# Kernel optimization log

Hardware: AMD Instinct MI355X
Metric: run time of the kernel (lower is better)

## Reference

```python
import jax, jax.numpy as jnp
import numpy as np

B, S, D_MODEL, N_HEADS = 4, 2048, 1024, 16
HEAD_DIM = D_MODEL // N_HEADS  # 64; used only for the softmax scale, as in the source


def setup_inputs() -> dict:
    key = jax.random.key(0)
    kq, kk, kv, kw = jax.random.split(key, 4)
    q = jax.random.normal(kq, (B, S, D_MODEL), dtype=jnp.float32)
    k = jax.random.normal(kk, (B, S, D_MODEL), dtype=jnp.float32)
    v = jax.random.normal(kv, (B, S, D_MODEL), dtype=jnp.float32)
    # out_proj: nn.Linear(d_model, d_model, bias=False) -> weight [out, in]
    W_out = jax.random.normal(kw, (D_MODEL, D_MODEL), dtype=jnp.float32) * (1.0 / np.sqrt(D_MODEL))
    return {"q": q, "k": k, "v": v, "W_out": W_out}


def reference(q, k, v, W_out):
    scale = 1.0 / jnp.sqrt(jnp.float32(HEAD_DIM))
    # scores: [B, Sq, Sk] -- full quadratic score matrix, as in the source
    scores = jnp.einsum("bqd,bkd->bqk", q, k) * scale
    attn = jax.nn.softmax(scores, axis=-1)
    out = jnp.einsum("bqk,bkd->bqd", attn, v)
    # torch Linear: y = x @ W^T
    return jnp.einsum("bsd,ed->bse", out, W_out)
```

## Files before the change

### kernel.cpp

```cpp
#include <hip/hip_runtime.h>
#include <hip/hip_fp16.h>
#include <stdint.h>

typedef _Float16 h16;
typedef _Float16 h16x8 __attribute__((ext_vector_type(8)));
typedef float f32x4 __attribute__((ext_vector_type(4)));

#define BB 4
#define SS 2048
#define DD 1024

#define EPI_H16 0
#define EPI_DIV 2

__device__ __forceinline__ void gload16(const void* g, void* l) {
    __builtin_amdgcn_global_load_lds(
        (const __attribute__((address_space(1))) uint32_t*)g,
        (__attribute__((address_space(3))) uint32_t*)l, 16, 0, 0);
}

__global__ __launch_bounds__(256) void cvt_qk(
    const float* __restrict__ q, const float* __restrict__ k,
    h16* __restrict__ qh, h16* __restrict__ kh, float* __restrict__ rowsum) {
    if (blockIdx.x == 0) {
#pragma unroll
        for (int i = 0; i < 32; ++i) rowsum[threadIdx.x + i * 256] = 0.f;
    }
    int b = blockIdx.x;
    const float* src; h16* dst; float sc = 1.0f;
    if (b < 1024)      { src = q; dst = qh; sc = 0.125f; }
    else               { src = k; dst = kh; b -= 1024; }
    size_t base = (size_t)b * 2048 + threadIdx.x;
    float4 a[8];
#pragma unroll
    for (int i = 0; i < 8; ++i) a[i] = ((const float4*)src)[base + (size_t)i * 256];
#pragma unroll
    for (int i = 0; i < 8; ++i) {
        union { int2 i2; h16 h[4]; } u;
        u.h[0] = (h16)(a[i].x * sc); u.h[1] = (h16)(a[i].y * sc);
        u.h[2] = (h16)(a[i].z * sc); u.h[3] = (h16)(a[i].w * sc);
        ((int2*)dst)[base + (size_t)i * 256] = u.i2;
    }
}

__device__ __forceinline__ void cvt_store(h16* dst, size_t g, float4 a) {
    union { int2 i2; h16 h[4]; } u;
    u.h[0] = (h16)a.x; u.h[1] = (h16)a.y; u.h[2] = (h16)a.z; u.h[3] = (h16)a.w;
    ((int2*)dst)[g] = u.i2;
}

__global__ __launch_bounds__(512, 2) void gemm1f(
    const h16* __restrict__ A, const h16* __restrict__ B, h16* __restrict__ C,
    const float* __restrict__ v, const float* __restrict__ w,
    h16* __restrict__ vh, h16* __restrict__ wh, float* __restrict__ rowsum)
{
    constexpr int ABYTES = 256 * 128;
    constexpr int BUFB   = 2 * ABYTES;
    __shared__ __align__(1024) char lds[2 * BUFB];

    const int tid = threadIdx.x;
    const int gid = blockIdx.x;
    const size_t tidg = (size_t)gid * 512 + tid;

    const int wgid = (gid & 7) * 32 + (gid >> 3);
    const int bb  = wgid / 64;
    const int rem = wgid % 64;
    const int tm = rem / 8, tn = rem % 8;
    const int row0 = tm * 256, col0 = tn * 256;

    const h16* Ab = A + (long long)bb * ((long long)SS * DD);
    const h16* Bb = B + (long long)bb * ((long long)SS * DD);

    const int lane = tid & 63, wid = tid >> 6;
    const int wm = wid >> 2, wn = wid & 3;
    const int frow = lane & 15, kq = lane >> 4;

    const int NT = DD >> 6;

    f32x4 acc[8][4];
#pragma unroll
    for (int m = 0; m < 8; ++m)
#pragma unroll
        for (int n = 0; n < 4; ++n) acc[m][n] = (f32x4){0.f, 0.f, 0.f, 0.f};

    char* l0 = (char*)lds;

    auto STAGE_B = [&](int kt, int buf) {
#pragma unroll
        for (int i = 0; i < 4; ++i) {
            int d = i * 512 + tid;
            int s = d & 7, r = d >> 3;
            int gg = s ^ (r & 7);
            gload16(Bb + (size_t)(col0 + r) * DD + kt + gg * 8,
                    l0 + buf * BUFB + ABYTES + (r * 8 + s) * 16);
        }
    };
    auto STAGE_AH = [&](int kt, int buf, int mh) {
#pragma unroll
        for (int i = 0; i < 2; ++i) {
            int d = i * 512 + tid;
            int s = d & 7, hr = d >> 3;
            int r = ((hr & ~63) << 1) + mh * 64 + (hr & 63);
            int gg = s ^ (r & 7);
            gload16(Ab + (size_t)(row0 + r) * DD + kt + gg * 8,
                    l0 + buf * BUFB + (r * 8 + s) * 16);
        }
    };
    auto READ_A = [&](int buf, int mh, h16x8 (&af)[4][2]) {
#pragma unroll
        for (int mm = 0; mm < 4; ++mm)
#pragma unroll
            for (int ks = 0; ks < 2; ++ks) {
                int r = wm * 128 + (mh * 4 + mm) * 16 + frow;
                int s = (ks * 4 + kq) ^ (r & 7);
                af[mm][ks] = *(const h16x8*)(l0 + buf * BUFB + (r * 8 + s) * 16);
            }
    };
    auto READ_B = [&](int buf, h16x8 (&bf)[4][2]) {
#pragma unroll
        for (int nn = 0; nn < 4; ++nn)
#pragma unroll
            for (int ks = 0; ks < 2; ++ks) {
                int r = wn * 64 + nn * 16 + frow;
                int s = (ks * 4 + kq) ^ (r & 7);
                bf[nn][ks] = *(const h16x8*)(l0 + buf * BUFB + ABYTES + (r * 8 + s) * 16);
            }
    };
    auto MFMA_H = [&](int mh, h16x8 (&af)[4][2], h16x8 (&bf)[4][2]) {
        __builtin_amdgcn_s_setprio(1);
#pragma unroll
        for (int ks = 0; ks < 2; ++ks)
#pragma unroll
            for (int mm = 0; mm < 4; ++mm)
#pragma unroll
                for (int nn = 0; nn < 4; ++nn)
                    acc[mh * 4 + mm][nn] =
                        __builtin_amdgcn_mfma_f32_16x16x32_f16(
                            af[mm][ks], bf[nn][ks], acc[mh * 4 + mm][nn], 0, 0, 0);
        __builtin_amdgcn_s_setprio(0);
    };

    {
        float4 w0 = ((const float4*)w)[tidg];
        float4 w1 = ((const float4*)w)[131072 + tidg];
        cvt_store(wh, tidg, w0);
        cvt_store(wh, 131072 + tidg, w1);
    }
    STAGE_B(0, 0); STAGE_AH(0, 0, 0); STAGE_AH(0, 0, 1);
    asm volatile("s_waitcnt vmcnt(2)" ::: "memory");
    __builtin_amdgcn_s_barrier();

    h16x8 af[4][2], bf[4][2];
    float4 vbuf;

    for (int G = 0; G < NT; ++G) {
        const int buf = G & 1;
        const int kt1 = (G + 1) << 6;
        float4 vnew = ((const float4*)v)[(size_t)G * 131072 + tidg];
        if (G > 0) cvt_store(vh, (size_t)(G - 1) * 131072 + tidg, vbuf);
        vbuf = vnew;
        if (G + 1 < NT) {
            STAGE_B(kt1, buf ^ 1);
            STAGE_AH(kt1, buf ^ 1, 0);
            STAGE_AH(kt1, buf ^ 1, 1);
        }
        READ_A(buf, 0, af);
        READ_B(buf, bf);
        MFMA_H(0, af, bf);
        if (G + 1 < NT) asm volatile("s_waitcnt vmcnt(8)" ::: "memory");
        else            asm volatile("s_waitcnt vmcnt(0)" ::: "memory");
        __builtin_amdgcn_s_barrier();
        READ_A(buf, 1, af);
        MFMA_H(1, af, bf);
        if (G + 1 >= NT) break;
        asm volatile("s_waitcnt vmcnt(2)" ::: "memory");
        __builtin_amdgcn_s_barrier();
    }
    cvt_store(vh, (size_t)(NT - 1) * 131072 + tidg, vbuf);

    h16* Cb = C + (long long)bb * ((long long)SS * SS);
    float* rs = rowsum + bb * SS;
    const int erow = row0 + wm * 128 + (lane >> 4) * 4;
    const int ecol = col0 + wn * 64 + (lane & 15);
#pragma unroll
    for (int m = 0; m < 8; ++m)
#pragma unroll
        for (int j = 0; j < 4; ++j) {
            const int row = erow + m * 16 + j;
            float p = 0.f;
#pragma unroll
            for (int n = 0; n < 4; ++n) {
                float e = __expf(acc[m][n][j] - 16.0f);
                Cb[(size_t)row * SS + (ecol + n * 16)] = (h16)e;
                p += e;
            }
            p += __shfl_xor(p, 1);
            p += __shfl_xor(p, 2);
            p += __shfl_xor(p, 4);
            p += __shfl_xor(p, 8);
            if ((lane & 15) == 0) atomicAdd(&rs[row], p);
        }
}

template<int EPI>
__global__ __launch_bounds__(256, 2) void gemm2p_sm(
    const h16* __restrict__ A, const h16* __restrict__ B, void* __restrict__ Cv,
    int lda, int ldb, int ldc, int K, int tilesN, int tilesMN,
    long long aBatch, long long bBatch, long long cBatch, const float* __restrict__ rowsum)
{
    constexpr int ABYTES = 128 * 128;
    constexpr int BBYTES = 128 * 128;
    constexpr int BUFB   = ABYTES + BBYTES;

    __shared__ __align__(1024) char lds[2 * BUFB];

    const int tid = threadIdx.x;
    const int nwg = gridDim.x;
    const int bid = blockIdx.x;
    const int wgid = (bid & 7) * (nwg >> 3) + (bid >> 3);
    const int bb  = wgid / tilesMN;
    const int rem = wgid % tilesMN;
    const int tm = rem / tilesN, tn = rem % tilesN;
    const int row0 = tm * 128, col0 = tn * 128;

    const h16* Ab = A + (long long)bb * aBatch;
    const h16* Bb = B + (long long)bb * bBatch;

    const int lane = tid & 63, wid = tid >> 6;
    const int wm = wid >> 1, wn = wid & 1;
    const int frow = lane & 15, kq = lane >> 4;

    const int NT = K >> 6;

    f32x4 acc[4][4];
#pragma unroll
    for (int m = 0; m < 4; ++m)
#pragma unroll
        for (int n = 0; n < 4; ++n) acc[m][n] = (f32x4){0.f, 0.f, 0.f, 0.f};

    char* l0 = (char*)lds;

    auto STAGE_B = [&](int kt, int buf) {
#pragma unroll
        for (int i = 0; i < 4; ++i) {
            int d = i * 256 + tid;
            int s = d & 7, r = d >> 3;
            int gg = s ^ (r & 7);
            gload16(Bb + (size_t)(col0 + r) * ldb + kt + gg * 8,
                    l0 + buf * BUFB + ABYTES + (r * 8 + s) * 16);
        }
    };
    auto STAGE_AH = [&](int kt, int buf, int mh) {
#pragma unroll
        for (int i = 0; i < 2; ++i) {
            int d = i * 256 + tid;
            int s = d & 7, hr = d >> 3;
            int r = ((hr & ~31) << 1) + mh * 32 + (hr & 31);
            int gg = s ^ (r & 7);
            gload16(Ab + (size_t)(row0 + r) * lda + kt + gg * 8,
                    l0 + buf * BUFB + (r * 8 + s) * 16);
        }
    };
    auto READ_A = [&](int buf, int mh, h16x8 (&af)[2][2]) {
#pragma unroll
        for (int mm = 0; mm < 2; ++mm)
#pragma unroll
            for (int ks = 0; ks < 2; ++ks) {
                int r = wm * 64 + (mh * 2 + mm) * 16 + frow;
                int s = (ks * 4 + kq) ^ (r & 7);
                af[mm][ks] = *(const h16x8*)(l0 + buf * BUFB + (r * 8 + s) * 16);
            }
    };
    auto READ_B = [&](int buf, h16x8 (&bf)[4][2]) {
#pragma unroll
        for (int nn = 0; nn < 4; ++nn)
#pragma unroll
            for (int ks = 0; ks < 2; ++ks) {
                int r = wn * 64 + nn * 16 + frow;
                int s = (ks * 4 + kq) ^ (r & 7);
                bf[nn][ks] = *(const h16x8*)(l0 + buf * BUFB + ABYTES + (r * 8 + s) * 16);
            }
    };
    auto MFMA_H = [&](int mh, h16x8 (&af)[2][2], h16x8 (&bf)[4][2]) {
        __builtin_amdgcn_s_setprio(1);
#pragma unroll
        for (int ks = 0; ks < 2; ++ks)
#pragma unroll
            for (int mm = 0; mm < 2; ++mm)
#pragma unroll
                for (int nn = 0; nn < 4; ++nn)
                    acc[mh * 2 + mm][nn] =
                        __builtin_amdgcn_mfma_f32_16x16x32_f16(
                            af[mm][ks], bf[nn][ks], acc[mh * 2 + mm][nn], 0, 0, 0);
        __builtin_amdgcn_s_setprio(0);
    };

    STAGE_B(0, 0); STAGE_AH(0, 0, 0); STAGE_AH(0, 0, 1);
    asm volatile("s_waitcnt vmcnt(2)" ::: "memory");
    __builtin_amdgcn_s_barrier();

    h16x8 af[2][2], bf[4][2];

    for (int G = 0; G < NT; ++G) {
        const int buf = G & 1;
        const int kt1 = (G + 1) << 6;
        if (G + 1 < NT) {
            STAGE_B(kt1, buf ^ 1);
            STAGE_AH(kt1, buf ^ 1, 0);
            STAGE_AH(kt1, buf ^ 1, 1);
        }
        READ_A(buf, 0, af);
        READ_B(buf, bf);
        MFMA_H(0, af, bf);
        if (G + 1 < NT) asm volatile("s_waitcnt vmcnt(8)" ::: "memory");
        else            asm volatile("s_waitcnt vmcnt(0)" ::: "memory");
        __builtin_amdgcn_s_barrier();
        READ_A(buf, 1, af);
        MFMA_H(1, af, bf);
        if (G + 1 >= NT) break;
        asm volatile("s_waitcnt vmcnt(2)" ::: "memory");
        __builtin_amdgcn_s_barrier();
    }

    const int erow = row0 + wm * 64 + (lane >> 4) * 4;
    const int ecol = col0 + wn * 64 + (lane & 15);
#pragma unroll
    for (int m = 0; m < 4; ++m)
#pragma unroll
        for (int n = 0; n < 4; ++n)
#pragma unroll
            for (int j = 0; j < 4; ++j) {
                int row = erow + m * 16 + j, col = ecol + n * 16;
                float vv = acc[m][n][j];
                if constexpr (EPI == EPI_DIV) {
                    float* C = (float*)Cv + (long long)bb * cBatch;
                    C[(size_t)row * ldc + col] = vv / rowsum[bb * SS + row];
                } else {
                    h16* C = (h16*)Cv + (long long)bb * cBatch;
                    C[(size_t)row * ldc + col] = (h16)vv;
                }
            }
}

extern "C" void kernel_launch(void* const* d_in, const int* in_sizes, int n_in,
                              void* d_out, int out_size, void* d_ws, size_t ws_size,
                              hipStream_t stream) {
    (void)in_sizes; (void)n_in; (void)out_size; (void)ws_size;
    const float* q = (const float*)d_in[0];
    const float* k = (const float*)d_in[1];
    const float* v = (const float*)d_in[2];
    const float* w = (const float*)d_in[3];
    float* out = (float*)d_out;

    const size_t QKV = (size_t)BB * SS * DD;
    h16* qh = (h16*)d_ws;
    h16* kh = qh + QKV;
    h16* vh = kh + QKV;
    h16* wh = vh + QKV;
    h16* sc = wh + (size_t)DD * DD;
    float* rowsum = (float*)(sc + (size_t)BB * SS * SS);

    cvt_qk<<<2048, 256, 0, stream>>>(q, k, qh, kh, rowsum);

    gemm1f<<<256, 512, 0, stream>>>(qh, kh, sc, v, w, vh, wh, rowsum);

    h16* vpT = qh;
    gemm2p_sm<EPI_H16><<<512, 256, 0, stream>>>(
        wh, vh, (void*)vpT, DD, DD, BB * SS, DD, 64, 512,
        0LL, 0LL, 0LL, nullptr);

    gemm2p_sm<EPI_DIV><<<512, 256, 0, stream>>>(
        sc, vpT, (void*)out, SS, BB * SS, DD, SS, 8, 128,
        (long long)SS * SS, (long long)SS, (long long)SS * DD, rowsum);
}
```

Baseline: 131.1 us.

## Shrink QK^T tiles to 128x128 and split V/W conversion into dedicated blocks

Reworks the first GEMM from 256 workgroups of 512 threads computing 256x256 tiles into 1024 workgroups of 256 threads computing 128x128 tiles. It also moves the fp32-to-fp16 conversion of V and W out of the GEMM main loop into 256 separate blocks launched alongside. The aim is to fill the GPU's CUs more evenly and stop the conversion traffic from interleaving with the MFMA pipeline. In exchange each tile loads more redundant A/B data from global memory, and the conversion blocks compete with the GEMM blocks for bandwidth.

```diff
diff --git a/kernel.cpp b/kernel.cpp
--- a/kernel.cpp
+++ b/kernel.cpp
@@ -49,37 +49,51 @@
     ((int2*)dst)[g] = u.i2;
 }
 
-__global__ __launch_bounds__(512, 2) void gemm1f(
+__global__ __launch_bounds__(256, 2) void g1sm(
     const h16* __restrict__ A, const h16* __restrict__ B, h16* __restrict__ C,
     const float* __restrict__ v, const float* __restrict__ w,
     h16* __restrict__ vh, h16* __restrict__ wh, float* __restrict__ rowsum)
 {
-    constexpr int ABYTES = 256 * 128;
+    constexpr int ABYTES = 128 * 128;
     constexpr int BUFB   = 2 * ABYTES;
     __shared__ __align__(1024) char lds[2 * BUFB];
 
     const int tid = threadIdx.x;
-    const int gid = blockIdx.x;
-    const size_t tidg = (size_t)gid * 512 + tid;
-
-    const int wgid = (gid & 7) * 32 + (gid >> 3);
-    const int bb  = wgid / 64;
-    const int rem = wgid % 64;
-    const int tm = rem / 8, tn = rem % 8;
-    const int row0 = tm * 256, col0 = tn * 256;
+
+    if (blockIdx.x < 256) {
+        const size_t lane = (size_t)blockIdx.x * 256 + tid;
+#pragma unroll 4
+        for (int i = 0; i < 32; ++i) {
+            size_t g = (size_t)i * 65536 + lane;
+            cvt_store(vh, g, ((const float4*)v)[g]);
+        }
+#pragma unroll
+        for (int i = 0; i < 4; ++i) {
+            size_t g = (size_t)i * 65536 + lane;
+            cvt_store(wh, g, ((const float4*)w)[g]);
+        }
+        return;
+    }
+
+    const int gid = blockIdx.x - 256;
+    const int wgid = (gid & 7) * 128 + (gid >> 3);
+    const int bb  = wgid / 256;
+    const int rem = wgid % 256;
+    const int tm = rem / 16, tn = rem % 16;
+    const int row0 = tm * 128, col0 = tn * 128;
 
     const h16* Ab = A + (long long)bb * ((long long)SS * DD);
     const h16* Bb = B + (long long)bb * ((long long)SS * DD);
 
     const int lane = tid & 63, wid = tid >> 6;
-    const int wm = wid >> 2, wn = wid & 3;
+    const int wm = wid >> 1, wn = wid & 1;
     const int frow = lane & 15, kq = lane >> 4;
 
     const int NT = DD >> 6;
 
-    f32x4 acc[8][4];
-#pragma unroll
-    for (int m = 0; m < 8; ++m)
+    f32x4 acc[4][4];
+#pragma unroll
+    for (int m = 0; m < 4; ++m)
 #pragma unroll
         for (int n = 0; n < 4; ++n) acc[m][n] = (f32x4){0.f, 0.f, 0.f, 0.f};
 
@@ -88,7 +102,7 @@
     auto STAGE_B = [&](int kt, int buf) {
 #pragma unroll
         for (int i = 0; i < 4; ++i) {
-            int d = i * 512 + tid;
+            int d = i * 256 + tid;
             int s = d & 7, r = d >> 3;
             int gg = s ^ (r & 7);
             gload16(Bb + (size_t)(col0 + r) * DD + kt + gg * 8,
@@ -98,20 +112,20 @@
     auto STAGE_AH = [&](int kt, int buf, int mh) {
 #pragma unroll
         for (int i = 0; i < 2; ++i) {
-            int d = i * 512 + tid;
+            int d = i * 256 + tid;
             int s = d & 7, hr = d >> 3;
-            int r = ((hr & ~63) << 1) + mh * 64 + (hr & 63);
+            int r = ((hr & ~31) << 1) + mh * 32 + (hr & 31);
             int gg = s ^ (r & 7);
             gload16(Ab + (size_t)(row0 + r) * DD + kt + gg * 8,
                     l0 + buf * BUFB + (r * 8 + s) * 16);
         }
     };
-    auto READ_A = [&](int buf, int mh, h16x8 (&af)[4][2]) {
-#pragma unroll
-        for (int mm = 0; mm < 4; ++mm)
+    auto READ_A = [&](int buf, int mh, h16x8 (&af)[2][2]) {
+#pragma unroll
+        for (int mm = 0; mm < 2; ++mm)
 #pragma unroll
             for (int ks = 0; ks < 2; ++ks) {
-                int r = wm * 128 + (mh * 4 + mm) * 16 + frow;
+                int r = wm * 64 + (mh * 2 + mm) * 16 + frow;
                 int s = (ks * 4 + kq) ^ (r & 7);
                 af[mm][ks] = *(const h16x8*)(l0 + buf * BUFB + (r * 8 + s) * 16);
             }
@@ -126,39 +140,29 @@
                 bf[nn][ks] = *(const h16x8*)(l0 + buf * BUFB + ABYTES + (r * 8 + s) * 16);
             }
     };
-    auto MFMA_H = [&](int mh, h16x8 (&af)[4][2], h16x8 (&bf)[4][2]) {
+    auto MFMA_H = [&](int mh, h16x8 (&af)[2][2], h16x8 (&bf)[4][2]) {
         __builtin_amdgcn_s_setprio(1);
 #pragma unroll
         for (int ks = 0; ks < 2; ++ks)
 #pragma unroll
-            for (int mm = 0; mm < 4; ++mm)
+            for (int mm = 0; mm < 2; ++mm)
 #pragma unroll
                 for (int nn = 0; nn < 4; ++nn)
-                    acc[mh * 4 + mm][nn] =
+                    acc[mh * 2 + mm][nn] =
                         __builtin_amdgcn_mfma_f32_16x16x32_f16(
-                            af[mm][ks], bf[nn][ks], acc[mh * 4 + mm][nn], 0, 0, 0);
+                            af[mm][ks], bf[nn][ks], acc[mh * 2 + mm][nn], 0, 0, 0);
         __builtin_amdgcn_s_setprio(0);
     };
 
-    {
-        float4 w0 = ((const float4*)w)[tidg];
-        float4 w1 = ((const float4*)w)[131072 + tidg];
-        cvt_store(wh, tidg, w0);
-        cvt_store(wh, 131072 + tidg, w1);
-    }
     STAGE_B(0, 0); STAGE_AH(0, 0, 0); STAGE_AH(0, 0, 1);
     asm volatile("s_waitcnt vmcnt(2)" ::: "memory");
     __builtin_amdgcn_s_barrier();
 
-    h16x8 af[4][2], bf[4][2];
-    float4 vbuf;
+    h16x8 af[2][2], bf[4][2];
 
     for (int G = 0; G < NT; ++G) {
         const int buf = G & 1;
         const int kt1 = (G + 1) << 6;
-        float4 vnew = ((const float4*)v)[(size_t)G * 131072 + tidg];
-        if (G > 0) cvt_store(vh, (size_t)(G - 1) * 131072 + tidg, vbuf);
-        vbuf = vnew;
         if (G + 1 < NT) {
             STAGE_B(kt1, buf ^ 1);
             STAGE_AH(kt1, buf ^ 1, 0);
@@ -176,14 +180,13 @@
         asm volatile("s_waitcnt vmcnt(2)" ::: "memory");
         __builtin_amdgcn_s_barrier();
     }
-    cvt_store(vh, (size_t)(NT - 1) * 131072 + tidg, vbuf);
 
     h16* Cb = C + (long long)bb * ((long long)SS * SS);
     float* rs = rowsum + bb * SS;
-    const int erow = row0 + wm * 128 + (lane >> 4) * 4;
+    const int erow = row0 + wm * 64 + (lane >> 4) * 4;
     const int ecol = col0 + wn * 64 + (lane & 15);
 #pragma unroll
-    for (int m = 0; m < 8; ++m)
+    for (int m = 0; m < 4; ++m)
 #pragma unroll
         for (int j = 0; j < 4; ++j) {
             const int row = erow + m * 16 + j;
@@ -362,7 +365,7 @@
 
     cvt_qk<<<2048, 256, 0, stream>>>(q, k, qh, kh, rowsum);
 
-    gemm1f<<<256, 512, 0, stream>>>(qh, kh, sc, v, w, vh, wh, rowsum);
+    g1sm<<<1280, 256, 0, stream>>>(qh, kh, sc, v, w, vh, wh, rowsum);
 
     h16* vpT = qh;
     gemm2p_sm<EPI_H16><<<512, 256, 0, stream>>>(
```

After: 138.8 us. 1.06x slower.
